# Kernel optimization log

Hardware: AMD Instinct MI355X
Metric: run time of the kernel (lower is better)

The kernel has to match this reference:

```python
import jax, jax.numpy as jnp
import numpy as np

VOCAB = 256
HID = 1024
LAYERS = 2


def setup_inputs() -> dict:
    key = jax.random.key(0)
    k_idx, k_emb, k_wi, k_wh, k_proj = jax.random.split(key, 5)
    B, T = 64, 512
    idx = jax.random.randint(k_idx, (B, T), 0, VOCAB, dtype=jnp.int32)
    s_emb = 1.0 / np.sqrt(HID)
    embed = jax.random.normal(k_emb, (VOCAB, HID), dtype=jnp.float32) * s_emb
    # flax LSTMCell: input dense (no bias) + recurrent dense (bias), gates [i,f,g,o]
    Wi = jax.random.normal(k_wi, (LAYERS, HID, 4 * HID), dtype=jnp.float32) * s_emb
    Wh = jax.random.normal(k_wh, (LAYERS, HID, 4 * HID), dtype=jnp.float32) * s_emb
    b = jnp.zeros((LAYERS, 4 * HID), dtype=jnp.float32)
    Wproj = jax.random.normal(k_proj, (HID, VOCAB), dtype=jnp.float32) * s_emb
    return {"idx": idx, "embed": embed, "Wi": Wi, "Wh": Wh, "b": b, "Wproj": Wproj}


def _lstm_forward(idx, embed, Wi, Wh, b, Wproj):
    x = embed[idx]                      # (B, T, H)
    B, T, H = x.shape
    L = Wi.shape[0]
    c0 = jnp.zeros((L, B, H), dtype=x.dtype)
    h0 = jnp.zeros((L, B, H), dtype=x.dtype)

    def step(carry, x_t):
        c, h = carry                    # each (L, B, H)
        inp = x_t                       # (B, H)
        cs, hs = [], []
        for l in range(L):              # fixed small layer loop
            z = inp @ Wi[l] + h[l] @ Wh[l] + b[l]   # (B, 4H)
            i, f, g, o = jnp.split(z, 4, axis=-1)
            i = jax.nn.sigmoid(i)
            f = jax.nn.sigmoid(f)
            g = jnp.tanh(g)
            o = jax.nn.sigmoid(o)
            c_new = f * c[l] + i * g
            h_new = o * jnp.tanh(c_new)
            inp = h_new                 # dropout rate 0 in eval mode
            cs.append(c_new)
            hs.append(h_new)
        return (jnp.stack(cs), jnp.stack(hs)), inp

    x_tm = jnp.swapaxes(x, 0, 1)        # (T, B, H) time-major
    _, hs_tm = jax.lax.scan(step, (c0, h0), x_tm)
    hs = jnp.swapaxes(hs_tm, 0, 1)      # (B, T, H)
    logits = hs @ Wproj                 # (B, T, V)
    return logits


def reference(idx, embed, Wi, Wh, b, Wproj):
    return _lstm_forward(idx, embed, Wi, Wh, b, Wproj)
```

## Files before the change

kernel.cpp:

```cpp
#include <hip/hip_runtime.h>

#define BB 64
#define HH 1024
#define TT 512
#define GG 4096
#define VV 256
#define NBLK 256
#define BPG 128
#define BG  32
#define UPB 8
#define SLOT (BB * HH)
#define GREG 32768

typedef __attribute__((ext_vector_type(8))) short short8;
typedef __attribute__((ext_vector_type(4))) float f32x4;
typedef __attribute__((ext_vector_type(4))) unsigned uint32x4;

__device__ __forceinline__ unsigned short f2bf(float f) {
  unsigned u = __float_as_uint(f);
  u += 0x7fffu + ((u >> 16) & 1u);
  return (unsigned short)(u >> 16);
}

__device__ __forceinline__ float sigf(float x) { return 1.0f / (1.0f + __expf(-x)); }
__device__ __forceinline__ float tanhfast(float x) {
  float t = __expf(2.0f * x);
  return (t - 1.0f) / (t + 1.0f);
}

__device__ __forceinline__ unsigned pkmax(unsigned a, unsigned b) {
  unsigned d;
  asm("v_pk_max_u16 %0, %1, %2" : "=v"(d) : "v"(a), "v"(b));
  return d;
}

__device__ __forceinline__ bool anypoison(uint32x4 a, uint32x4 b) {
  const unsigned mm = pkmax(pkmax(pkmax(a[0], a[1]), pkmax(a[2], a[3])),
                            pkmax(pkmax(b[0], b[1]), pkmax(b[2], b[3])));
  return ((mm & 0xFFFFu) == 0xFFFFu) || ((mm >> 16) == 0xFFFFu);
}

__device__ __forceinline__ short8 as_s8(uint32x4 v) {
  short8 r;
  __builtin_memcpy(&r, &v, 16);
  return r;
}

__global__ void __launch_bounds__(256, 1)
p0_kernel(const float* __restrict__ embed, const float* __restrict__ Wi,
          const float* __restrict__ bias, float* __restrict__ P0p)
{
  __shared__ float elds[16][1024];
  const int tid = threadIdx.x;
  const int vt = blockIdx.x >> 4;
  const int ct = blockIdx.x & 15;
  for (int i = tid; i < 16 * 1024; i += 256)
    elds[i >> 10][i & 1023] = embed[((vt * 16 + (i >> 10)) << 10) + (i & 1023)];
  __syncthreads();
  const int c = ct * 256 + tid;
  float acc[16];
#pragma unroll
  for (int v = 0; v < 16; ++v) acc[v] = 0.f;
  for (int kk = 0; kk < 1024; ++kk) {
    const float wv = Wi[kk * GG + c];
#pragma unroll
    for (int v = 0; v < 16; ++v) acc[v] = fmaf(elds[v][kk], wv, acc[v]);
  }
  const int u = c & 1023, g = c >> 10;
  const float bv = bias[c];
#pragma unroll
  for (int v = 0; v < 16; ++v)
    P0p[(((size_t)(vt * 16 + v) * HH) + u) * 4 + g] = acc[v] + bv;
}

__global__ void pack_misc(const float* __restrict__ Wproj, const float* __restrict__ bias,
                          unsigned short* __restrict__ Wppk, float* __restrict__ b1p)
{
  const int t = blockIdx.x * 256 + threadIdx.x;
  if (t < 16 * 32 * 64) {
    const int lane = t & 63;
    const int kt = (t >> 6) & 31;
    const int nt = t >> 11;
    const int v = nt * 16 + (lane & 15);
    const int kb = kt * 32 + (lane >> 4) * 8;
    short8 fr;
#pragma unroll
    for (int e = 0; e < 8; ++e)
      fr[e] = (short)f2bf(Wproj[(size_t)(kb + e) * VV + v]);
    *(short8*)(Wppk + (size_t)t * 8) = fr;
  }
  if (t < 4096)
    b1p[t] = bias[GG + (t & 3) * HH + (t >> 2)];
}

__global__ void __launch_bounds__(256, 1)
lstm_persist(const float* __restrict__ Wi, const float* __restrict__ Wh,
             const int* __restrict__ idx, const float* __restrict__ P0p,
             const float* __restrict__ b1p,
             unsigned short* __restrict__ h0r, unsigned short* __restrict__ hs)
{
  __shared__ short wlds[32][2][64][8];
  __shared__ float zbuf[2][4][32][36];
  __shared__ unsigned short hstage[2][256];

  const int tid = threadIdx.x;
  const int lane = tid & 63;
  const int w = tid >> 6;
  const int bid = blockIdx.x;
  const int g = bid & 1;
  const int ub = bid >> 1;
  const int w8 = w * 8;

  short8 wi1r[8][2], wh1r[8][2];
  {
    const int arow16 = lane & 15;
    const int kb4 = (lane >> 4) * 8;
    for (int kk = 0; kk < 8; ++kk) {
      const int kbase = (w8 + kk) * 32 + kb4;
      for (int nt = 0; nt < 2; ++nt) {
        const int cl = nt * 16 + arow16;
        const int cg = (cl & 3) * HH + ub * UPB + (cl >> 2);
        short8 fr;
#pragma unroll
        for (int e = 0; e < 8; ++e)
          fr[e] = (short)f2bf(Wh[(size_t)(kbase + e) * GG + cg]);
        *(short8*)(&wlds[w8 + kk][nt][lane][0]) = fr;
      }
    }
    const float* srcWi1 = Wi + (size_t)HH * GG;
    const float* srcWh1 = Wh + (size_t)HH * GG;
#pragma unroll
    for (int kk = 0; kk < 8; ++kk) {
      const int kbase = (w8 + kk) * 32 + kb4;
#pragma unroll
      for (int nt = 0; nt < 2; ++nt) {
        const int cl = nt * 16 + arow16;
        const int cg = (cl & 3) * HH + ub * UPB + (cl >> 2);
        short8 fa, fb;
#pragma unroll
        for (int e = 0; e < 8; ++e) {
          fa[e] = (short)f2bf(srcWi1[(size_t)(kbase + e) * GG + cg]);
          fb[e] = (short)f2bf(srcWh1[(size_t)(kbase + e) * GG + cg]);
        }
        wi1r[kk][nt] = fa;
        wh1r[kk][nt] = fb;
      }
    }
  }
  __syncthreads();

  const int ebl = tid >> 3;
  const int eu = tid & 7;
  const int ebg = g * BG + ebl;
  const int egu = ub * UPB + eu;
  float c0 = 0.f, c1 = 0.f;
  const float4 b1v = *(const float4*)(b1p + egu * 4);

  const int arow = lane & 15;
  const int ro0 = g * GREG + w8 * 1024 + (lane >> 4) * 256 + arow * 8;
  const int ro1 = ro0 + 128;

  int v_pf = idx[ebg * TT];
  float4 p_pf = *(const float4*)(P0p + ((size_t)v_pf * HH + egu) * 4);

#define GLDP(dst, addr)                                                        \
  asm volatile("global_load_dwordx4 %0, %1, off sc0 sc1"                       \
               : "=&v"(dst) : "v"(addr));

#define WAITV0                                                                 \
  asm volatile("s_waitcnt vmcnt(0)" ::: "memory");                             \
  __builtin_amdgcn_sched_barrier(0);

#define LDB(s, nt) (*(const short8*)(&wlds[w8 + (s)][nt][lane][0]))

#define CHK(s)                                                                 \
  if (need & (1u << (s))) {                                                    \
    if (__any(anypoison(ring[s][0], ring[s][1]))) nneed |= (1u << (s));        \
  }

#define REISSUE(s, pa, pb)                                                     \
  if (need & (1u << (s))) {                                                    \
    GLDP(ring[s][0], (pa) + (s) * 1024)                                        \
    GLDP(ring[s][1], (pb) + (s) * 1024)                                        \
  }

#define DATAPOLL(pa, pb)                                                       \
  {                                                                            \
    GLDP(ring[0][0], (pa) + 0 * 1024) GLDP(ring[0][1], (pb) + 0 * 1024)        \
    GLDP(ring[1][0], (pa) + 1 * 1024) GLDP(ring[1][1], (pb) + 1 * 1024)        \
    GLDP(ring[2][0], (pa) + 2 * 1024) GLDP(ring[2][1], (pb) + 2 * 1024)        \
    GLDP(ring[3][0], (pa) + 3 * 1024) GLDP(ring[3][1], (pb) + 3 * 1024)        \
    GLDP(ring[4][0], (pa) + 4 * 1024) GLDP(ring[4][1], (pb) + 4 * 1024)        \
    GLDP(ring[5][0], (pa) + 5 * 1024) GLDP(ring[5][1], (pb) + 5 * 1024)        \
    GLDP(ring[6][0], (pa) + 6 * 1024) GLDP(ring[6][1], (pb) + 6 * 1024)        \
    GLDP(ring[7][0], (pa) + 7 * 1024) GLDP(ring[7][1], (pb) + 7 * 1024)        \
    unsigned need = 0xFFu;                                                     \
    int tries = 0;                                                             \
    for (;;) {                                                                 \
      WAITV0                                                                   \
      unsigned nneed = 0;                                                      \
      CHK(0) CHK(1) CHK(2) CHK(3) CHK(4) CHK(5) CHK(6) CHK(7)                  \
      need = nneed;                                                            \
      if (!need) break;                                                        \
      if (++tries > (1 << 17)) break;                        \
      __builtin_amdgcn_s_sleep(4);                                             \
      REISSUE(0, pa, pb) REISSUE(1, pa, pb) REISSUE(2, pa, pb)                 \
      REISSUE(3, pa, pb) REISSUE(4, pa, pb) REISSUE(5, pa, pb)                 \
      REISSUE(6, pa, pb) REISSUE(7, pa, pb)                                    \
    }                                                                          \
    __builtin_amdgcn_sched_barrier(0);                                         \
  }

#define STAGE_A01(s)                                                           \
  {                                                                            \
    const short8 n0a = LDB(((s) + 1) & 7, 0);                                  \
    const short8 n0b = LDB(((s) + 1) & 7, 1);                                  \
    const short8 rA = as_s8(ring[s][0]);                                       \
    const short8 rB = as_s8(ring[s][1]);                                       \
    a0[0][0] = __builtin_amdgcn_mfma_f32_16x16x32_bf16(rA, f0a, a0[0][0], 0, 0, 0); \
    a0[0][1] = __builtin_amdgcn_mfma_f32_16x16x32_bf16(rA, f0b, a0[0][1], 0, 0, 0); \
    a0[1][0] = __builtin_amdgcn_mfma_f32_16x16x32_bf16(rB, f0a, a0[1][0], 0, 0, 0); \
    a0[1][1] = __builtin_amdgcn_mfma_f32_16x16x32_bf16(rB, f0b, a0[1][1], 0, 0, 0); \
    a1[0][0] = __builtin_amdgcn_mfma_f32_16x16x32_bf16(rA, wi1r[s][0], a1[0][0], 0, 0, 0); \
    a1[0][1] = __builtin_amdgcn_mfma_f32_16x16x32_bf16(rA, wi1r[s][1], a1[0][1], 0, 0, 0); \
    a1[1][0] = __builtin_amdgcn_mfma_f32_16x16x32_bf16(rB, wi1r[s][0], a1[1][0], 0, 0, 0); \
    a1[1][1] = __builtin_amdgcn_mfma_f32_16x16x32_bf16(rB, wi1r[s][1], a1[1][1], 0, 0, 0); \
    f0a = n0a; f0b = n0b;                                                      \
  }

#define STAGE_A2(s)                                                            \
  {                                                                            \
    const short8 rA = as_s8(ring[s][0]);                                       \
    const short8 rB = as_s8(ring[s][1]);                                       \
    a1[0][0] = __builtin_amdgcn_mfma_f32_16x16x32_bf16(rA, wh1r[s][0], a1[0][0], 0, 0, 0); \
    a1[0][1] = __builtin_amdgcn_mfma_f32_16x16x32_bf16(rA, wh1r[s][1], a1[0][1], 0, 0, 0); \
    a1[1][0] = __builtin_amdgcn_mfma_f32_16x16x32_bf16(rB, wh1r[s][0], a1[1][0], 0, 0, 0); \
    a1[1][1] = __builtin_amdgcn_mfma_f32_16x16x32_bf16(rB, wh1r[s][1], a1[1][1], 0, 0, 0); \
  }

  for (int k = 0; k <= TT; ++k) {
    const unsigned short* A01 = h0r + (size_t)k * SLOT;
    const unsigned short* A2  = hs + (size_t)(k > 0 ? (k - 1) : 0) * SLOT;
    const unsigned short* p00 = A01 + ro0;
    const unsigned short* p01 = A01 + ro1;
    const unsigned short* p10 = A2 + ro0;
    const unsigned short* p11 = A2 + ro1;

    f32x4 a0[2][2], a1[2][2];
#pragma unroll
    for (int mt = 0; mt < 2; ++mt)
#pragma unroll
      for (int nt = 0; nt < 2; ++nt) {
        a0[mt][nt] = f32x4{0.f, 0.f, 0.f, 0.f};
        a1[mt][nt] = f32x4{0.f, 0.f, 0.f, 0.f};
      }

    uint32x4 ring[8][2];

    DATAPOLL(p00, p01)
    {
      short8 f0a = LDB(0, 0), f0b = LDB(0, 1);
      STAGE_A01(0) STAGE_A01(1) STAGE_A01(2) STAGE_A01(3)
      STAGE_A01(4) STAGE_A01(5) STAGE_A01(6) STAGE_A01(7)
    }

    {
      const int colb = lane & 15;
      const int r0w = (lane >> 4) * 4;
#pragma unroll
      for (int mt = 0; mt < 2; ++mt)
#pragma unroll
        for (int nt = 0; nt < 2; ++nt)
#pragma unroll
          for (int r = 0; r < 4; ++r)
            zbuf[0][w][mt * 16 + r0w + r][nt * 16 + colb] = a0[mt][nt][r];
    }
    __syncthreads();
    {
      float z0[4] = {0.f, 0.f, 0.f, 0.f};
#pragma unroll
      for (int ww = 0; ww < 4; ++ww) {
        const float4 pv = *(const float4*)(&zbuf[0][ww][ebl][eu * 4]);
        z0[0] += pv.x; z0[1] += pv.y; z0[2] += pv.z; z0[3] += pv.w;
      }
      if (k < TT) {
        const float gi = sigf(z0[0] + p_pf.x);
        const float gf = sigf(z0[1] + p_pf.y);
        const float gc = tanhfast(z0[2] + p_pf.z);
        const float go = sigf(z0[3] + p_pf.w);
        c0 = gf * c0 + gi * gc;
        hstage[0][ebl * 8 + eu] = f2bf(go * tanhfast(c0));
        if (k + 1 < TT) {
          v_pf = idx[ebg * TT + k + 1];
          p_pf = *(const float4*)(P0p + ((size_t)v_pf * HH + egu) * 4);
        }
      }
    }
    __syncthreads();

    if (w == 0 && k < TT && lane < 32) {
      unsigned short* dst = h0r + (size_t)(k + 1) * SLOT + g * GREG + ub * 256 + lane * 8;
      const uint32x4 val = *(const uint32x4*)&hstage[0][lane * 8];
      asm volatile("global_store_dwordx4 %0, %1, off sc0 sc1"
                   :: "v"(dst), "v"(val) : "memory");
    }

    DATAPOLL(p10, p11)
    STAGE_A2(0) STAGE_A2(1) STAGE_A2(2) STAGE_A2(3)
    STAGE_A2(4) STAGE_A2(5) STAGE_A2(6) STAGE_A2(7)

    {
      const int colb = lane & 15;
      const int r0w = (lane >> 4) * 4;
#pragma unroll
      for (int mt = 0; mt < 2; ++mt)
#pragma unroll
        for (int nt = 0; nt < 2; ++nt)
#pragma unroll
          for (int r = 0; r < 4; ++r)
            zbuf[1][w][mt * 16 + r0w + r][nt * 16 + colb] = a1[mt][nt][r];
    }
    __syncthreads();
    if (k > 0) {
      float z1[4] = {0.f, 0.f, 0.f, 0.f};
#pragma unroll
      for (int ww = 0; ww < 4; ++ww) {
        const float4 pv = *(const float4*)(&zbuf[1][ww][ebl][eu * 4]);
        z1[0] += pv.x; z1[1] += pv.y; z1[2] += pv.z; z1[3] += pv.w;
      }
      const float gi = sigf(z1[0] + b1v.x);
      const float gf = sigf(z1[1] + b1v.y);
      const float gc = tanhfast(z1[2] + b1v.z);
      const float go = sigf(z1[3] + b1v.w);
      c1 = gf * c1 + gi * gc;
      hstage[1][ebl * 8 + eu] = f2bf(go * tanhfast(c1));
    }
    __syncthreads();

    if (w == 0 && k > 0 && lane < 32) {
      unsigned short* dst = hs + (size_t)k * SLOT + g * GREG + ub * 256 + lane * 8;
      const uint32x4 val = *(const uint32x4*)&hstage[1][lane * 8];
      asm volatile("global_store_dwordx4 %0, %1, off sc0 sc1"
                   :: "v"(dst), "v"(val) : "memory");
    }
  }

  asm volatile("s_waitcnt vmcnt(0)" ::: "memory");
#undef GLDP
#undef WAITV0
#undef LDB
#undef CHK
#undef REISSUE
#undef DATAPOLL
#undef STAGE_A01
#undef STAGE_A2
}

__global__ void __launch_bounds__(256, 1)
proj_kernel(const unsigned short* __restrict__ hs, const unsigned short* __restrict__ Wppk,
            float* __restrict__ out)
{
  __shared__ short blds[16][64][8];
  const int tid = threadIdx.x;
  const int lane = tid & 63;
  const int w = tid >> 6;
  const int t = blockIdx.x;
  const unsigned short* A = hs + (size_t)(t + 1) * SLOT;
  f32x4 acc[16];
#pragma unroll
  for (int nt = 0; nt < 16; ++nt) acc[nt] = f32x4{0.f, 0.f, 0.f, 0.f};
  const int brow = w * 16 + (lane & 15);
  const int gp = brow >> 5;
  const int bl = brow & 31;
  const int aoff = gp * GREG + (lane >> 4) * 256 + bl * 8;
  for (int kt = 0; kt < 32; ++kt) {
    __syncthreads();
    for (int i = tid; i < 16 * 64; i += 256)
      *(short8*)(&blds[i >> 6][i & 63][0]) =
          *(const short8*)(Wppk + (size_t)(((i >> 6) * 32 + kt) * 64 + (i & 63)) * 8);
    __syncthreads();
    const short8 a = *(const short8*)(A + aoff + kt * 1024);
#pragma unroll
    for (int nt = 0; nt < 16; ++nt) {
      const short8 bf = *(const short8*)(&blds[nt][lane][0]);
      acc[nt] = __builtin_amdgcn_mfma_f32_16x16x32_bf16(a, bf, acc[nt], 0, 0, 0);
    }
  }
#pragma unroll
  for (int nt = 0; nt < 16; ++nt) {
#pragma unroll
    for (int r = 0; r < 4; ++r) {
      const int bbv = w * 16 + (lane >> 4) * 4 + r;
      const int vv = nt * 16 + (lane & 15);
      out[((size_t)bbv * TT + t) * VV + vv] = acc[nt][r];
    }
  }
}

extern "C" void kernel_launch(void* const* d_in, const int* in_sizes, int n_in,
                              void* d_out, int out_size, void* d_ws, size_t ws_size,
                              hipStream_t stream)
{
  (void)in_sizes; (void)n_in; (void)out_size; (void)ws_size;
  const int* idx = (const int*)d_in[0];
  const float* embed = (const float*)d_in[1];
  const float* Wi = (const float*)d_in[2];
  const float* Wh = (const float*)d_in[3];
  const float* bias = (const float*)d_in[4];
  const float* Wproj = (const float*)d_in[5];
  float* out = (float*)d_out;

  char* ws = (char*)d_ws;
  size_t off = 0;
  unsigned short* h0r = (unsigned short*)(ws + off); off += 513ull * SLOT * 2;
  unsigned short* hs = (unsigned short*)(ws + off);  off += 513ull * SLOT * 2;
  float* P0p = (float*)(ws + off);                  off += 256ull * HH * 4 * 4;
  unsigned short* Wppk = (unsigned short*)(ws + off); off += 16ull * 32 * 64 * 8 * 2;
  float* b1p = (float*)(ws + off);                  off += 4096ull * 4;

  hipMemsetAsync(h0r, 0xFF, 513ull * SLOT * 2, stream);
  hipMemsetAsync(hs, 0xFF, 513ull * SLOT * 2, stream);
  hipMemsetAsync(h0r, 0, (size_t)SLOT * 2, stream);
  hipMemsetAsync(hs, 0, (size_t)SLOT * 2, stream);

  p0_kernel<<<256, 256, 0, stream>>>(embed, Wi, bias, P0p);
  pack_misc<<<128, 256, 0, stream>>>(Wproj, bias, Wppk, b1p);

  lstm_persist<<<NBLK, 256, 0, stream>>>(Wi, Wh, idx, P0p, b1p, h0r, hs);

  proj_kernel<<<512, 256, 0, stream>>>(hs, Wppk, out);
}
```

Measured before the change: 2.446 ms.

## Double-buffer poll rings to prefetch next-step hidden-state loads early

Splits the single register ring into two rings: the layer-0 ring for the next timestep is issued at the end of each iteration, and the layer-1 ring is issued at the start, before layer-0 data is consumed. Partial vmcnt waits let the loads overlap with compute and synchronisation instead of being issued and waited on serially. Poison checks and reissues still handle data that was not ready yet. The cost is extra register pressure from a second 16-vector ring and more reissues when the prefetch fires before producers have written.

Measured after the change: 2.225 ms. 1.1x faster.

```diff
diff --git a/kernel.cpp b/kernel.cpp
--- a/kernel.cpp
+++ b/kernel.cpp
@@ -167,46 +167,54 @@
   asm volatile("global_load_dwordx4 %0, %1, off sc0 sc1"                       \
                : "=&v"(dst) : "v"(addr));
 
-#define WAITV0                                                                 \
-  asm volatile("s_waitcnt vmcnt(0)" ::: "memory");                             \
+#define WAITI(n)                                                               \
+  asm volatile("s_waitcnt vmcnt(" #n ")" ::: "memory");                        \
   __builtin_amdgcn_sched_barrier(0);
 
 #define LDB(s, nt) (*(const short8*)(&wlds[w8 + (s)][nt][lane][0]))
 
-#define CHK(s)                                                                 \
+#define ISSUE_RING(rg, pa, pb)                                                 \
+  GLDP(rg[0][0], (pa) + 0 * 1024) GLDP(rg[0][1], (pb) + 0 * 1024)              \
+  GLDP(rg[1][0], (pa) + 1 * 1024) GLDP(rg[1][1], (pb) + 1 * 1024)              \
+  GLDP(rg[2][0], (pa) + 2 * 1024) GLDP(rg[2][1], (pb) + 2 * 1024)              \
+  GLDP(rg[3][0], (pa) + 3 * 1024) GLDP(rg[3][1], (pb) + 3 * 1024)              \
+  GLDP(rg[4][0], (pa) + 4 * 1024) GLDP(rg[4][1], (pb) + 4 * 1024)              \
+  GLDP(rg[5][0], (pa) + 5 * 1024) GLDP(rg[5][1], (pb) + 5 * 1024)              \
+  GLDP(rg[6][0], (pa) + 6 * 1024) GLDP(rg[6][1], (pb) + 6 * 1024)              \
+  GLDP(rg[7][0], (pa) + 7 * 1024) GLDP(rg[7][1], (pb) + 7 * 1024)
+
+#define CHKR(rg, s)                                                            \
   if (need & (1u << (s))) {                                                    \
-    if (__any(anypoison(ring[s][0], ring[s][1]))) nneed |= (1u << (s));        \
-  }
-
-#define REISSUE(s, pa, pb)                                                     \
+    if (__any(anypoison(rg[s][0], rg[s][1]))) nneed |= (1u << (s));            \
+  }
+
+#define REISS(rg, s, pa, pb)                                                   \
   if (need & (1u << (s))) {                                                    \
-    GLDP(ring[s][0], (pa) + (s) * 1024)                                        \
-    GLDP(ring[s][1], (pb) + (s) * 1024)                                        \
-  }
-
-#define DATAPOLL(pa, pb)                                                       \
+    GLDP(rg[s][0], (pa) + (s) * 1024)                                          \
+    GLDP(rg[s][1], (pb) + (s) * 1024)                                          \
+  }
+
+#define SCANLOOP(rg, pa, pb)                                                   \
   {                                                                            \
-    GLDP(ring[0][0], (pa) + 0 * 1024) GLDP(ring[0][1], (pb) + 0 * 1024)        \
-    GLDP(ring[1][0], (pa) + 1 * 1024) GLDP(ring[1][1], (pb) + 1 * 1024)        \
-    GLDP(ring[2][0], (pa) + 2 * 1024) GLDP(ring[2][1], (pb) + 2 * 1024)        \
-    GLDP(ring[3][0], (pa) + 3 * 1024) GLDP(ring[3][1], (pb) + 3 * 1024)        \
-    GLDP(ring[4][0], (pa) + 4 * 1024) GLDP(ring[4][1], (pb) + 4 * 1024)        \
-    GLDP(ring[5][0], (pa) + 5 * 1024) GLDP(ring[5][1], (pb) + 5 * 1024)        \
-    GLDP(ring[6][0], (pa) + 6 * 1024) GLDP(ring[6][1], (pb) + 6 * 1024)        \
-    GLDP(ring[7][0], (pa) + 7 * 1024) GLDP(ring[7][1], (pb) + 7 * 1024)        \
     unsigned need = 0xFFu;                                                     \
+    {                                                                          \
+      unsigned nneed = 0;                                                      \
+      CHKR(rg, 0) CHKR(rg, 1) CHKR(rg, 2) CHKR(rg, 3)                          \
+      CHKR(rg, 4) CHKR(rg, 5) CHKR(rg, 6) CHKR(rg, 7)                          \
+      need = nneed;                                                            \
+    }                                                                          \
     int tries = 0;                                                             \
-    for (;;) {                                                                 \
-      WAITV0                                                                   \
-      unsigned nneed = 0;                                                      \
-      CHK(0) CHK(1) CHK(2) CHK(3) CHK(4) CHK(5) CHK(6) CHK(7)                  \
-      need = nneed;                                                            \
-      if (!need) break;                                                        \
+    while (need) {                                                             \
       if (++tries > (1 << 17)) break;                        \
       __builtin_amdgcn_s_sleep(4);                                             \
-      REISSUE(0, pa, pb) REISSUE(1, pa, pb) REISSUE(2, pa, pb)                 \
-      REISSUE(3, pa, pb) REISSUE(4, pa, pb) REISSUE(5, pa, pb)                 \
-      REISSUE(6, pa, pb) REISSUE(7, pa, pb)                                    \
+      REISS(rg, 0, pa, pb) REISS(rg, 1, pa, pb) REISS(rg, 2, pa, pb)           \
+      REISS(rg, 3, pa, pb) REISS(rg, 4, pa, pb) REISS(rg, 5, pa, pb)           \
+      REISS(rg, 6, pa, pb) REISS(rg, 7, pa, pb)                                \
+      WAITI(0)                                                                 \
+      unsigned nneed = 0;                                                      \
+      CHKR(rg, 0) CHKR(rg, 1) CHKR(rg, 2) CHKR(rg, 3)                          \
+      CHKR(rg, 4) CHKR(rg, 5) CHKR(rg, 6) CHKR(rg, 7)                          \
+      need = nneed;                                                            \
     }                                                                          \
     __builtin_amdgcn_sched_barrier(0);                                         \
   }
@@ -215,8 +223,8 @@
   {                                                                            \
     const short8 n0a = LDB(((s) + 1) & 7, 0);                                  \
     const short8 n0b = LDB(((s) + 1) & 7, 1);                                  \
-    const short8 rA = as_s8(ring[s][0]);                                       \
-    const short8 rB = as_s8(ring[s][1]);                                       \
+    const short8 rA = as_s8(ringA[s][0]);                                      \
+    const short8 rB = as_s8(ringA[s][1]);                                      \
     a0[0][0] = __builtin_amdgcn_mfma_f32_16x16x32_bf16(rA, f0a, a0[0][0], 0, 0, 0); \
     a0[0][1] = __builtin_amdgcn_mfma_f32_16x16x32_bf16(rA, f0b, a0[0][1], 0, 0, 0); \
     a0[1][0] = __builtin_amdgcn_mfma_f32_16x16x32_bf16(rB, f0a, a0[1][0], 0, 0, 0); \
@@ -230,21 +238,34 @@
 
 #define STAGE_A2(s)                                                            \
   {                                                                            \
-    const short8 rA = as_s8(ring[s][0]);                                       \
-    const short8 rB = as_s8(ring[s][1]);                                       \
+    const short8 rA = as_s8(ringB[s][0]);                                      \
+    const short8 rB = as_s8(ringB[s][1]);                                      \
     a1[0][0] = __builtin_amdgcn_mfma_f32_16x16x32_bf16(rA, wh1r[s][0], a1[0][0], 0, 0, 0); \
     a1[0][1] = __builtin_amdgcn_mfma_f32_16x16x32_bf16(rA, wh1r[s][1], a1[0][1], 0, 0, 0); \
     a1[1][0] = __builtin_amdgcn_mfma_f32_16x16x32_bf16(rB, wh1r[s][0], a1[1][0], 0, 0, 0); \
     a1[1][1] = __builtin_amdgcn_mfma_f32_16x16x32_bf16(rB, wh1r[s][1], a1[1][1], 0, 0, 0); \
   }
 
+  uint32x4 ringA[8][2];
+  uint32x4 ringB[8][2];
+
+  {
+    const unsigned short* pa = h0r + ro0;
+    const unsigned short* pb = h0r + ro1;
+    ISSUE_RING(ringA, pa, pb)
+  }
+
   for (int k = 0; k <= TT; ++k) {
-    const unsigned short* A01 = h0r + (size_t)k * SLOT;
-    const unsigned short* A2  = hs + (size_t)(k > 0 ? (k - 1) : 0) * SLOT;
-    const unsigned short* p00 = A01 + ro0;
-    const unsigned short* p01 = A01 + ro1;
-    const unsigned short* p10 = A2 + ro0;
-    const unsigned short* p11 = A2 + ro1;
+    const unsigned short* pa0 = h0r + (size_t)k * SLOT + ro0;
+    const unsigned short* pb0 = h0r + (size_t)k * SLOT + ro1;
+    const unsigned short* pa1 = hs + (size_t)(k > 0 ? (k - 1) : 0) * SLOT + ro0;
+    const unsigned short* pb1 = hs + (size_t)(k > 0 ? (k - 1) : 0) * SLOT + ro1;
+
+    ISSUE_RING(ringB, pa1, pb1)
+
+    WAITI(16)
+
+    SCANLOOP(ringA, pa0, pb0)
 
     f32x4 a0[2][2], a1[2][2];
 #pragma unroll
@@ -255,9 +276,6 @@
         a1[mt][nt] = f32x4{0.f, 0.f, 0.f, 0.f};
       }
 
-    uint32x4 ring[8][2];
-
-    DATAPOLL(p00, p01)
     {
       short8 f0a = LDB(0, 0), f0b = LDB(0, 1);
       STAGE_A01(0) STAGE_A01(1) STAGE_A01(2) STAGE_A01(3)
@@ -305,7 +323,9 @@
                    :: "v"(dst), "v"(val) : "memory");
     }
 
-    DATAPOLL(p10, p11)
+    if (w == 0) { WAITI(1) } else { WAITI(0) }
+    SCANLOOP(ringB, pa1, pb1)
+
     STAGE_A2(0) STAGE_A2(1) STAGE_A2(2) STAGE_A2(3)
     STAGE_A2(4) STAGE_A2(5) STAGE_A2(6) STAGE_A2(7)
 
@@ -343,15 +363,22 @@
       asm volatile("global_store_dwordx4 %0, %1, off sc0 sc1"
                    :: "v"(dst), "v"(val) : "memory");
     }
+
+    if (k < TT) {
+      const unsigned short* na = h0r + (size_t)(k + 1) * SLOT + ro0;
+      const unsigned short* nb = h0r + (size_t)(k + 1) * SLOT + ro1;
+      ISSUE_RING(ringA, na, nb)
+    }
   }
 
   asm volatile("s_waitcnt vmcnt(0)" ::: "memory");
 #undef GLDP
-#undef WAITV0
+#undef WAITI
 #undef LDB
-#undef CHK
-#undef REISSUE
-#undef DATAPOLL
+#undef ISSUE_RING
+#undef CHKR
+#undef REISS
+#undef SCANLOOP
 #undef STAGE_A01
 #undef STAGE_A2
 }
```
